# Kernel optimization log

Measured on AMD Instinct MI355X. Metric: run time of the kernel, lower is better.

Reference implementation:

```python
import jax, jax.numpy as jnp
import numpy as np

B, L, E = 512, 50, 512
VOCAB = 32000
EPS = 1e-5


def setup_inputs() -> dict:
    key = jax.random.key(0)
    ks = jax.random.split(key, 16)
    inp = {
        'src_tokens': jax.random.randint(ks[0], (B, L), 0, VOCAB, dtype=jnp.int32),
        'trg_tokens': jax.random.randint(ks[1], (B, L), 0, VOCAB, dtype=jnp.int32),
        'pad_idx': 1,
        'emb_src': jax.random.normal(ks[2], (VOCAB, E), jnp.float32) * 0.02,
        'emb_trg': jax.random.normal(ks[3], (VOCAB, E), jnp.float32) * 0.02,
        'W1': jax.random.normal(ks[4], (20, E), jnp.float32) / np.sqrt(E),  # Conv1d(1,20,k=E) kernel squeezed
        'b1': jax.random.normal(ks[5], (20,), jnp.float32) * 0.01,
        'g1': jnp.ones((20,), jnp.float32),
        'beta1': jnp.zeros((20,), jnp.float32),
        'W2': jax.random.normal(ks[6], (40, 20, 3, 3), jnp.float32) / np.sqrt(20 * 9),
        'b2': jax.random.normal(ks[7], (40,), jnp.float32) * 0.01,
        'g2': jnp.ones((40,), jnp.float32),
        'beta2': jnp.zeros((40,), jnp.float32),
        'Wfc1': jax.random.normal(ks[8], (20, 40 * 11 * 11), jnp.float32) / np.sqrt(40 * 11 * 11),
        'bfc1': jnp.zeros((20,), jnp.float32),
        'Wfc2': jax.random.normal(ks[9], (1, 20), jnp.float32) / np.sqrt(20),
        'bfc2': jnp.zeros((1,), jnp.float32),
    }
    return inp


def _maxpool2(x):  # [B,C,H,W] -> 2x2/2 valid max pool
    return jax.lax.reduce_window(x, -jnp.inf, jax.lax.max, (1, 1, 2, 2), (1, 1, 2, 2), 'VALID')


def reference(src_tokens, trg_tokens, pad_idx, emb_src, emb_trg, W1, b1, g1, beta1,
              W2, b2, g2, beta2, Wfc1, bfc1, Wfc2, bfc2):
    src_e = emb_src[src_tokens]  # [B,L,E]
    trg_e = emb_trg[trg_tokens]  # [B,L,E]

    def conv1_bn_relu(x):
        # per-sample Conv1d(1,20,k=E): collapses E -> scalar per position/channel
        f = jnp.einsum('ble,ce->blc', x, W1) + b1  # [B,L,20]
        # per-sample BatchNorm1d in training mode: stats over the L positions of each sample
        mu = jnp.mean(f, axis=1, keepdims=True)
        var = jnp.var(f, axis=1, keepdims=True)  # biased, as torch uses for normalization
        f = (f - mu) * jax.lax.rsqrt(var + EPS) * g1 + beta1
        return jax.nn.relu(f)

    s = conv1_bn_relu(src_e)  # [B,L,20]
    t = conv1_bn_relu(trg_e)  # [B,L,20]

    # broadcast outer-sum: out[b,i,j,c] = s[b,j,c] + t[b,i,c]
    out = s[:, None, :, :] + t[:, :, None, :]          # [B,L,L,20]
    out = jnp.transpose(out, (0, 3, 1, 2))             # [B,20,L,L]
    out = _maxpool2(out)                                # [B,20,25,25]

    out = jax.lax.conv_general_dilated(out, W2, (1, 1), 'VALID') + b2[None, :, None, None]  # [B,40,23,23]
    # BatchNorm2d training mode: stats over (batch, H, W)
    mu = jnp.mean(out, axis=(0, 2, 3), keepdims=True)
    var = jnp.var(out, axis=(0, 2, 3), keepdims=True)
    out = (out - mu) * jax.lax.rsqrt(var + EPS) * g2[None, :, None, None] + beta2[None, :, None, None]
    out = jax.nn.relu(out)
    out = _maxpool2(out)                                # [B,40,11,11]

    out = out.reshape(out.shape[0], -1)                 # [B,4840]
    out = out @ Wfc1.T + bfc1
    out = out @ Wfc2.T + bfc2
    return jax.nn.sigmoid(out)                          # [B,1]
```

## Files before the change

kernel.cpp:

```cpp
#include <hip/hip_runtime.h>
#include <hip/hip_bf16.h>

#define EPS 1e-5f

__device__ __forceinline__ float bf2f(unsigned short u) {
  union { unsigned int i; float f; } x; x.i = ((unsigned int)u) << 16; return x.f;
}
__device__ __forceinline__ float loadp(const void* p, int i, bool f32) {
  return f32 ? ((const float*)p)[i] : bf2f(((const unsigned short*)p)[i]);
}
__device__ __forceinline__ bool detect_f32(const void* g1) {
  return ((const unsigned int*)g1)[0] == 0x3F800000u;
}

__global__ __launch_bounds__(256) void k0_prep(
    const void* __restrict__ W1, const void* __restrict__ W2,
    const void* __restrict__ Wfc1,
    const void* __restrict__ g1, const void* __restrict__ beta1,
    const void* __restrict__ g2, const void* __restrict__ beta2,
    const void* __restrict__ bfc1, const void* __restrict__ Wfc2,
    const void* __restrict__ bfc2,
    float* __restrict__ W1T, float* __restrict__ WT, float* __restrict__ WS,
    float* __restrict__ Wfc1T, float* __restrict__ prm)
{
  const bool f32 = detect_f32(g1);
  int g = blockIdx.x * 256 + threadIdx.x;
  const int NT = 64 * 256;
  for (int i = g; i < 512 * 20; i += NT) {
    int e = i / 20, c = i - e * 20;
    W1T[i] = loadp(W1, c * 512 + e, f32);
  }
  for (int i = g; i < 40 * 3 * 20; i += NT) {
    int o = i / 60, r = i - o * 60;
    int k = r / 20, c = r - k * 20;
    float st = 0.f, ss = 0.f;
    for (int q = 0; q < 3; ++q) {
      st += loadp(W2, ((o * 20 + c) * 3 + k) * 3 + q, f32);
      ss += loadp(W2, ((o * 20 + c) * 3 + q) * 3 + k, f32);
    }
    WT[(o * 3 + k) * 20 + c] = st;
    WS[(o * 3 + k) * 20 + c] = ss;
  }
  for (int i = g; i < 4840 * 20; i += NT) {
    int idx = i / 20, kk = i - idx * 20;
    Wfc1T[i] = loadp(Wfc1, kk * 4840 + idx, f32);
  }
  if (g < 20)        prm[g]       = loadp(g1,    g,        f32);
  else if (g < 40)   prm[g]       = loadp(beta1, g - 20,   f32);
  else if (g < 80)   prm[g]       = loadp(g2,    g - 40,   f32);
  else if (g < 120)  prm[g]       = loadp(beta2, g - 80,   f32);
  else if (g < 140)  prm[g]       = loadp(bfc1,  g - 120,  f32);
  else if (g < 160)  prm[g]       = loadp(Wfc2,  g - 140,  f32);
  else if (g == 160) prm[g]       = loadp(bfc2,  0,        f32);
}

__global__ __launch_bounds__(256) void k1_gemv(
    const int* __restrict__ src_tok, const int* __restrict__ trg_tok,
    const void* __restrict__ emb_src, const void* __restrict__ emb_trg,
    const void* __restrict__ g1flag,
    const float* __restrict__ W1T,
    float* __restrict__ f)
{
  const bool f32 = detect_f32(g1flag);
  int m = blockIdx.x * 256 + threadIdx.x;
  int side = (m >= 25600);
  int r = m - side * 25600;
  int tok = side ? trg_tok[r] : src_tok[r];
  const void* emb = side ? emb_trg : emb_src;
  float acc[20];
#pragma unroll
  for (int c = 0; c < 20; ++c) acc[c] = 0.f;
  if (f32) {
    const float4* row = (const float4*)((const float*)emb + (size_t)tok * 512);
    for (int ec = 0; ec < 64; ++ec) {
      float4 q0 = row[2 * ec], q1 = row[2 * ec + 1];
      float v[8] = { q0.x, q0.y, q0.z, q0.w, q1.x, q1.y, q1.z, q1.w };
      const float* w = W1T + ec * 160;
#pragma unroll
      for (int j = 0; j < 8; ++j)
#pragma unroll
        for (int c = 0; c < 20; ++c)
          acc[c] = fmaf(v[j], w[j * 20 + c], acc[c]);
    }
  } else {
    const unsigned short* row = (const unsigned short*)emb + (size_t)tok * 512;
    for (int ec = 0; ec < 64; ++ec) {
      uint4 q = *(const uint4*)(row + ec * 8);
      const unsigned int* qu = (const unsigned int*)&q;
      float v[8];
#pragma unroll
      for (int j = 0; j < 4; ++j) {
        union { unsigned int i; float f; } lo, hi;
        lo.i = qu[j] << 16; hi.i = qu[j] & 0xffff0000u;
        v[2 * j] = lo.f; v[2 * j + 1] = hi.f;
      }
      const float* w = W1T + ec * 160;
#pragma unroll
      for (int j = 0; j < 8; ++j)
#pragma unroll
        for (int c = 0; c < 20; ++c)
          acc[c] = fmaf(v[j], w[j * 20 + c], acc[c]);
    }
  }
  float* out = f + (size_t)m * 20;
#pragma unroll
  for (int c = 0; c < 20; ++c) out[c] = acc[c];
}

__global__ __launch_bounds__(256) void k2_bnconv(
    const float* __restrict__ f,
    const float* __restrict__ WT, const float* __restrict__ WS,
    const float* __restrict__ prm,
    float* __restrict__ C1)
{
  __shared__ float fl[1000];
  __shared__ float wl[2400];
  __shared__ float pmax[500];
  __shared__ float sc[20], sh[20];
  int bb = blockIdx.x;
  int side = bb >> 9, b = bb & 511;
  int t = threadIdx.x;
  const float* fsrc = f + (size_t)(side * 25600 + b * 50) * 20;
  for (int i = t; i < 1000; i += 256) fl[i] = fsrc[i];
  const float* wsrc = side ? WT : WS;
  for (int i = t; i < 2400; i += 256) wl[i] = wsrc[i];
  __syncthreads();
  if (t < 20) {
    float s = 0.f, s2 = 0.f;
#pragma unroll
    for (int l = 0; l < 50; ++l) { float v = fl[l * 20 + t]; s += v; s2 += v * v; }
    float mu = s * (1.0f / 50.0f);
    float var = s2 * (1.0f / 50.0f) - mu * mu;
    float k = prm[t] * rsqrtf(var + EPS);
    sc[t] = k; sh[t] = prm[20 + t] - k * mu;
  }
  __syncthreads();
  for (int i = t; i < 500; i += 256) {
    int p = i / 20, c = i - p * 20;
    float k = sc[c], s0 = sh[c];
    float v0 = fmaxf(k * fl[(2 * p) * 20 + c] + s0, 0.f);
    float v1 = fmaxf(k * fl[(2 * p + 1) * 20 + c] + s0, 0.f);
    pmax[i] = fmaxf(v0, v1);
  }
  __syncthreads();
  float* out = C1 + (size_t)bb * 920;
  for (int i = t; i < 920; i += 256) {
    int o = i / 23, y = i - o * 23;
    float a = 0.f;
#pragma unroll
    for (int ky = 0; ky < 3; ++ky) {
      const float* wr = &wl[(o * 3 + ky) * 20];
      const float* pr = &pmax[(y + ky) * 20];
#pragma unroll
      for (int c = 0; c < 20; ++c) a = fmaf(wr[c], pr[c], a);
    }
    out[i] = a;
  }
}

__global__ __launch_bounds__(256) void k3_bn2stats(
    const float* __restrict__ C1,
    const float* __restrict__ prm,
    float* __restrict__ bn2)
{
  int o = blockIdx.x;
  int t = threadIdx.x;
  float s1a = 0, s2a = 0, s1b = 0, s2b = 0, sab = 0;
  for (int b = t; b < 512; b += 256) {
    const float* pa = C1 + ((size_t)(512 + b) * 40 + o) * 23;
    const float* pb = C1 + ((size_t)b * 40 + o) * 23;
    float ra = 0, rb = 0;
#pragma unroll
    for (int y = 0; y < 23; ++y) {
      float va = pa[y]; ra += va; s2a += va * va;
      float vb = pb[y]; rb += vb; s2b += vb * vb;
    }
    s1a += ra; s1b += rb; sab += ra * rb;
  }
  __shared__ float R[5][256];
  R[0][t] = s1a; R[1][t] = s2a; R[2][t] = s1b; R[3][t] = s2b; R[4][t] = sab;
  __syncthreads();
  for (int s = 128; s > 0; s >>= 1) {
    if (t < s) {
#pragma unroll
      for (int q = 0; q < 5; ++q) R[q][t] += R[q][t + s];
    }
    __syncthreads();
  }
  if (t == 0) {
    const float invN = 1.0f / (512.0f * 23.0f);
    float muA = R[0][0] * invN, muB = R[2][0] * invN;
    float ea2 = R[1][0] * invN - muA * muA;
    float eb2 = R[3][0] * invN - muB * muB;
    float cross = 2.0f * (R[4][0] * (1.0f / (529.0f * 512.0f)) - muA * muB);
    float var = ea2 + eb2 + cross;
    float k = prm[40 + o] * rsqrtf(var + EPS);
    bn2[o] = k;
    bn2[40 + o] = prm[80 + o] - k * (muA + muB);
  }
}

__global__ __launch_bounds__(256) void k4_fc(
    const float* __restrict__ C1,
    const float* __restrict__ bn2,
    const float* __restrict__ Wfc1T,
    const float* __restrict__ prm,
    const void* __restrict__ g1flag,
    void* __restrict__ outv)
{
  const bool f32 = detect_f32(g1flag);
  int b = blockIdx.x, t = threadIdx.x;
  __shared__ float mA[440], mB[440];
  __shared__ float k2s[40], c2s[40];
  __shared__ float red[20][256];
  __shared__ float o1[20];
  if (t < 40) k2s[t] = bn2[t];
  else if (t < 80) c2s[t - 40] = bn2[t];
  __syncthreads();
  for (int i = t; i < 440; i += 256) {
    int o = i / 11, y = i - o * 11;
    const float* pa = C1 + ((size_t)(512 + b) * 40 + o) * 23;
    const float* pb = C1 + ((size_t)b * 40 + o) * 23;
    float a0 = pa[2 * y], a1 = pa[2 * y + 1];
    float b0 = pb[2 * y], b1 = pb[2 * y + 1];
    if (k2s[o] >= 0.f) { mA[i] = fmaxf(a0, a1); mB[i] = fmaxf(b0, b1); }
    else               { mA[i] = fminf(a0, a1); mB[i] = fminf(b0, b1); }
  }
  __syncthreads();
  float acc[20];
#pragma unroll
  for (int c = 0; c < 20; ++c) acc[c] = 0.f;
  for (int idx = t; idx < 4840; idx += 256) {
    int o = idx / 121, r = idx - o * 121;
    int y = r / 11, x = r - y * 11;
    float p = fmaxf(k2s[o] * (mA[o * 11 + y] + mB[o * 11 + x]) + c2s[o], 0.f);
    const float* w = Wfc1T + idx * 20;
#pragma unroll
    for (int c = 0; c < 20; ++c) acc[c] = fmaf(p, w[c], acc[c]);
  }
#pragma unroll
  for (int c = 0; c < 20; ++c) red[c][t] = acc[c];
  __syncthreads();
  for (int s = 128; s > 0; s >>= 1) {
    if (t < s) {
#pragma unroll
      for (int c = 0; c < 20; ++c) red[c][t] += red[c][t + s];
    }
    __syncthreads();
  }
  if (t < 20) o1[t] = red[t][0] + prm[120 + t];
  __syncthreads();
  if (t == 0) {
    float z = prm[160];
#pragma unroll
    for (int c = 0; c < 20; ++c) z = fmaf(prm[140 + c], o1[c], z);
    float sg = 1.0f / (1.0f + expf(-z));
    if (f32) ((float*)outv)[b] = sg;
    else     ((__hip_bfloat16*)outv)[b] = __float2bfloat16(sg);
  }
}

extern "C" void kernel_launch(void* const* d_in, const int* in_sizes, int n_in,
                              void* d_out, int out_size, void* d_ws, size_t ws_size,
                              hipStream_t stream) {
  const int* src_tok = (const int*)d_in[0];
  const int* trg_tok = (const int*)d_in[1];
  const void* emb_src = d_in[3];
  const void* emb_trg = d_in[4];
  const void* W1    = d_in[5];
  const void* g1    = d_in[7];
  const void* beta1 = d_in[8];
  const void* W2    = d_in[9];
  const void* g2    = d_in[11];
  const void* beta2 = d_in[12];
  const void* Wfc1  = d_in[13];
  const void* bfc1  = d_in[14];
  const void* Wfc2  = d_in[15];
  const void* bfc2  = d_in[16];

  char* ws = (char*)d_ws;
  float* W1T   = (float*)(ws + 0);
  float* WT    = (float*)(ws + 40960);
  float* WS    = (float*)(ws + 50560);
  float* Wfc1T = (float*)(ws + 60160);
  float* prm   = (float*)(ws + 447360);
  float* bn2   = (float*)(ws + 448384);
  float* f     = (float*)(ws + 448896);
  float* C1    = (float*)(ws + 4544896);

  k0_prep<<<64, 256, 0, stream>>>(W1, W2, Wfc1, g1, beta1, g2, beta2, bfc1, Wfc2,
                                  bfc2, W1T, WT, WS, Wfc1T, prm);
  k1_gemv<<<200, 256, 0, stream>>>(src_tok, trg_tok, emb_src, emb_trg, g1, W1T, f);
  k2_bnconv<<<1024, 256, 0, stream>>>(f, WT, WS, prm, C1);
  k3_bn2stats<<<40, 256, 0, stream>>>(C1, prm, bn2);
  k4_fc<<<512, 256, 0, stream>>>(C1, bn2, Wfc1T, prm, g1, d_out);
}
```

Baseline: 242.2 us.

## Split embedding GEMV across waves and precompute BN2 partial sums in conv kernel

The embedding GEMV now assigns 8 waves per 64 tokens, each wave reducing a 64-element slice of E, with partials summed through shared memory. This raises parallelism from 200 blocks to 800. The conv kernel now writes per-sample channel sums and sums of squares, so the BN2 stats kernel reduces small arrays instead of rereading all of C1. C1 is stored channel-major, and the Wfc1 transpose in prep reads coalesced. The cost is extra shared memory and a sync in the GEMV, plus scattered C1 writes.

```diff
diff --git a/kernel.cpp b/kernel.cpp
--- a/kernel.cpp
+++ b/kernel.cpp
@@ -42,27 +42,31 @@
     WS[(o * 3 + k) * 20 + c] = ss;
   }
   for (int i = g; i < 4840 * 20; i += NT) {
-    int idx = i / 20, kk = i - idx * 20;
-    Wfc1T[i] = loadp(Wfc1, kk * 4840 + idx, f32);
-  }
-  if (g < 20)        prm[g]       = loadp(g1,    g,        f32);
-  else if (g < 40)   prm[g]       = loadp(beta1, g - 20,   f32);
-  else if (g < 80)   prm[g]       = loadp(g2,    g - 40,   f32);
-  else if (g < 120)  prm[g]       = loadp(beta2, g - 80,   f32);
-  else if (g < 140)  prm[g]       = loadp(bfc1,  g - 120,  f32);
-  else if (g < 160)  prm[g]       = loadp(Wfc2,  g - 140,  f32);
-  else if (g == 160) prm[g]       = loadp(bfc2,  0,        f32);
-}
-
-__global__ __launch_bounds__(256) void k1_gemv(
+    int kk = i / 4840, idx = i - kk * 4840;
+    Wfc1T[idx * 20 + kk] = loadp(Wfc1, i, f32);
+  }
+  if (g < 20)        prm[g] = loadp(g1,    g,       f32);
+  else if (g < 40)   prm[g] = loadp(beta1, g - 20,  f32);
+  else if (g < 80)   prm[g] = loadp(g2,    g - 40,  f32);
+  else if (g < 120)  prm[g] = loadp(beta2, g - 80,  f32);
+  else if (g < 140)  prm[g] = loadp(bfc1,  g - 120, f32);
+  else if (g < 160)  prm[g] = loadp(Wfc2,  g - 140, f32);
+  else if (g == 160) prm[g] = loadp(bfc2,  0,       f32);
+}
+
+__global__ __launch_bounds__(512) void k1_gemv(
     const int* __restrict__ src_tok, const int* __restrict__ trg_tok,
     const void* __restrict__ emb_src, const void* __restrict__ emb_trg,
     const void* __restrict__ g1flag,
     const float* __restrict__ W1T,
     float* __restrict__ f)
 {
+  __shared__ float part[8 * 64 * 21];
   const bool f32 = detect_f32(g1flag);
-  int m = blockIdx.x * 256 + threadIdx.x;
+  int t = threadIdx.x;
+  int lane = t & 63;
+  int ch = __builtin_amdgcn_readfirstlane(t >> 6);
+  int m = blockIdx.x * 64 + lane;
   int side = (m >= 25600);
   int r = m - side * 25600;
   int tok = side ? trg_tok[r] : src_tok[r];
@@ -71,22 +75,21 @@
 #pragma unroll
   for (int c = 0; c < 20; ++c) acc[c] = 0.f;
   if (f32) {
-    const float4* row = (const float4*)((const float*)emb + (size_t)tok * 512);
-    for (int ec = 0; ec < 64; ++ec) {
-      float4 q0 = row[2 * ec], q1 = row[2 * ec + 1];
-      float v[8] = { q0.x, q0.y, q0.z, q0.w, q1.x, q1.y, q1.z, q1.w };
-      const float* w = W1T + ec * 160;
-#pragma unroll
-      for (int j = 0; j < 8; ++j)
-#pragma unroll
-        for (int c = 0; c < 20; ++c)
-          acc[c] = fmaf(v[j], w[j * 20 + c], acc[c]);
+    const float4* rowp = (const float4*)((const float*)emb + (size_t)tok * 512 + ch * 64);
+    for (int q = 0; q < 16; ++q) {
+      float4 v4 = rowp[q];
+      float v[4] = { v4.x, v4.y, v4.z, v4.w };
+      const float* w = W1T + (ch * 64 + q * 4) * 20;
+#pragma unroll
+      for (int j = 0; j < 4; ++j)
+#pragma unroll
+        for (int c = 0; c < 20; ++c) acc[c] = fmaf(v[j], w[j * 20 + c], acc[c]);
     }
   } else {
-    const unsigned short* row = (const unsigned short*)emb + (size_t)tok * 512;
-    for (int ec = 0; ec < 64; ++ec) {
-      uint4 q = *(const uint4*)(row + ec * 8);
-      const unsigned int* qu = (const unsigned int*)&q;
+    const uint4* rowp = (const uint4*)((const unsigned short*)emb + (size_t)tok * 512 + ch * 64);
+    for (int q = 0; q < 8; ++q) {
+      uint4 u = rowp[q];
+      const unsigned int* qu = (const unsigned int*)&u;
       float v[8];
 #pragma unroll
       for (int j = 0; j < 4; ++j) {
@@ -94,33 +97,42 @@
         lo.i = qu[j] << 16; hi.i = qu[j] & 0xffff0000u;
         v[2 * j] = lo.f; v[2 * j + 1] = hi.f;
       }
-      const float* w = W1T + ec * 160;
+      const float* w = W1T + (ch * 64 + q * 8) * 20;
 #pragma unroll
       for (int j = 0; j < 8; ++j)
 #pragma unroll
-        for (int c = 0; c < 20; ++c)
-          acc[c] = fmaf(v[j], w[j * 20 + c], acc[c]);
-    }
-  }
-  float* out = f + (size_t)m * 20;
-#pragma unroll
-  for (int c = 0; c < 20; ++c) out[c] = acc[c];
+        for (int c = 0; c < 20; ++c) acc[c] = fmaf(v[j], w[j * 20 + c], acc[c]);
+    }
+  }
+  float* pp = &part[(ch * 64 + lane) * 21];
+#pragma unroll
+  for (int c = 0; c < 20; ++c) pp[c] = acc[c];
+  __syncthreads();
+  float* fout = f + (size_t)blockIdx.x * 1280;
+  for (int i = t; i < 1280; i += 512) {
+    int row = i / 20, c = i - row * 20;
+    float s = 0.f;
+#pragma unroll
+    for (int c2 = 0; c2 < 8; ++c2) s += part[(c2 * 64 + row) * 21 + c];
+    fout[i] = s;
+  }
 }
 
 __global__ __launch_bounds__(256) void k2_bnconv(
     const float* __restrict__ f,
     const float* __restrict__ WT, const float* __restrict__ WS,
     const float* __restrict__ prm,
-    float* __restrict__ C1)
+    float* __restrict__ C1, float* __restrict__ R, float* __restrict__ S2)
 {
   __shared__ float fl[1000];
   __shared__ float wl[2400];
   __shared__ float pmax[500];
   __shared__ float sc[20], sh[20];
+  __shared__ float convl[40 * 24];
   int bb = blockIdx.x;
-  int side = bb >> 9, b = bb & 511;
+  int side = bb >> 9;
   int t = threadIdx.x;
-  const float* fsrc = f + (size_t)(side * 25600 + b * 50) * 20;
+  const float* fsrc = f + (size_t)bb * 1000;
   for (int i = t; i < 1000; i += 256) fl[i] = fsrc[i];
   const float* wsrc = side ? WT : WS;
   for (int i = t; i < 2400; i += 256) wl[i] = wsrc[i];
@@ -143,7 +155,6 @@
     pmax[i] = fmaxf(v0, v1);
   }
   __syncthreads();
-  float* out = C1 + (size_t)bb * 920;
   for (int i = t; i < 920; i += 256) {
     int o = i / 23, y = i - o * 23;
     float a = 0.f;
@@ -154,45 +165,48 @@
 #pragma unroll
       for (int c = 0; c < 20; ++c) a = fmaf(wr[c], pr[c], a);
     }
-    out[i] = a;
-  }
-}
-
-__global__ __launch_bounds__(256) void k3_bn2stats(
-    const float* __restrict__ C1,
+    C1[((size_t)o * 1024 + bb) * 23 + y] = a;
+    convl[o * 24 + y] = a;
+  }
+  __syncthreads();
+  if (t < 40) {
+    float s = 0.f, s2 = 0.f;
+#pragma unroll
+    for (int y = 0; y < 23; ++y) { float v = convl[t * 24 + y]; s += v; s2 += v * v; }
+    R[t * 1024 + bb] = s;
+    S2[t * 1024 + bb] = s2;
+  }
+}
+
+__global__ __launch_bounds__(256) void k3_bn2(
+    const float* __restrict__ R, const float* __restrict__ S2,
     const float* __restrict__ prm,
     float* __restrict__ bn2)
 {
-  int o = blockIdx.x;
-  int t = threadIdx.x;
+  int o = blockIdx.x, t = threadIdx.x;
   float s1a = 0, s2a = 0, s1b = 0, s2b = 0, sab = 0;
   for (int b = t; b < 512; b += 256) {
-    const float* pa = C1 + ((size_t)(512 + b) * 40 + o) * 23;
-    const float* pb = C1 + ((size_t)b * 40 + o) * 23;
-    float ra = 0, rb = 0;
-#pragma unroll
-    for (int y = 0; y < 23; ++y) {
-      float va = pa[y]; ra += va; s2a += va * va;
-      float vb = pb[y]; rb += vb; s2b += vb * vb;
-    }
+    float ra = R[o * 1024 + 512 + b], rb = R[o * 1024 + b];
     s1a += ra; s1b += rb; sab += ra * rb;
-  }
-  __shared__ float R[5][256];
-  R[0][t] = s1a; R[1][t] = s2a; R[2][t] = s1b; R[3][t] = s2b; R[4][t] = sab;
+    s2a += S2[o * 1024 + 512 + b];
+    s2b += S2[o * 1024 + b];
+  }
+  __shared__ float Rd[5][256];
+  Rd[0][t] = s1a; Rd[1][t] = s2a; Rd[2][t] = s1b; Rd[3][t] = s2b; Rd[4][t] = sab;
   __syncthreads();
   for (int s = 128; s > 0; s >>= 1) {
     if (t < s) {
 #pragma unroll
-      for (int q = 0; q < 5; ++q) R[q][t] += R[q][t + s];
+      for (int q = 0; q < 5; ++q) Rd[q][t] += Rd[q][t + s];
     }
     __syncthreads();
   }
   if (t == 0) {
     const float invN = 1.0f / (512.0f * 23.0f);
-    float muA = R[0][0] * invN, muB = R[2][0] * invN;
-    float ea2 = R[1][0] * invN - muA * muA;
-    float eb2 = R[3][0] * invN - muB * muB;
-    float cross = 2.0f * (R[4][0] * (1.0f / (529.0f * 512.0f)) - muA * muB);
+    float muA = Rd[0][0] * invN, muB = Rd[2][0] * invN;
+    float ea2 = Rd[1][0] * invN - muA * muA;
+    float eb2 = Rd[3][0] * invN - muB * muB;
+    float cross = 2.0f * (Rd[4][0] * (1.0f / (529.0f * 512.0f)) - muA * muB);
     float var = ea2 + eb2 + cross;
     float k = prm[40 + o] * rsqrtf(var + EPS);
     bn2[o] = k;
@@ -219,8 +233,8 @@
   __syncthreads();
   for (int i = t; i < 440; i += 256) {
     int o = i / 11, y = i - o * 11;
-    const float* pa = C1 + ((size_t)(512 + b) * 40 + o) * 23;
-    const float* pb = C1 + ((size_t)b * 40 + o) * 23;
+    const float* pa = C1 + ((size_t)o * 1024 + 512 + b) * 23;
+    const float* pb = C1 + ((size_t)o * 1024 + b) * 23;
     float a0 = pa[2 * y], a1 = pa[2 * y + 1];
     float b0 = pb[2 * y], b1 = pb[2 * y + 1];
     if (k2s[o] >= 0.f) { mA[i] = fmaxf(a0, a1); mB[i] = fmaxf(b0, b1); }
@@ -285,13 +299,15 @@
   float* Wfc1T = (float*)(ws + 60160);
   float* prm   = (float*)(ws + 447360);
   float* bn2   = (float*)(ws + 448384);
-  float* f     = (float*)(ws + 448896);
-  float* C1    = (float*)(ws + 4544896);
+  float* R     = (float*)(ws + 448896);
+  float* S2    = (float*)(ws + 612736);
+  float* f     = (float*)(ws + 776576);
+  float* C1    = (float*)(ws + 4872576);
 
   k0_prep<<<64, 256, 0, stream>>>(W1, W2, Wfc1, g1, beta1, g2, beta2, bfc1, Wfc2,
                                   bfc2, W1T, WT, WS, Wfc1T, prm);
-  k1_gemv<<<200, 256, 0, stream>>>(src_tok, trg_tok, emb_src, emb_trg, g1, W1T, f);
-  k2_bnconv<<<1024, 256, 0, stream>>>(f, WT, WS, prm, C1);
-  k3_bn2stats<<<40, 256, 0, stream>>>(C1, prm, bn2);
+  k1_gemv<<<800, 512, 0, stream>>>(src_tok, trg_tok, emb_src, emb_trg, g1, W1T, f);
+  k2_bnconv<<<1024, 256, 0, stream>>>(f, WT, WS, prm, C1, R, S2);
+  k3_bn2<<<40, 256, 0, stream>>>(R, S2, prm, bn2);
   k4_fc<<<512, 256, 0, stream>>>(C1, bn2, Wfc1T, prm, g1, d_out);
 }
```

After: 287.4 us. 1.19x slower.
